# Kernel optimization log

Measured on AMD Instinct MI355X. Metric: run time of the kernel, lower is better.

## Reference

```python
import jax, jax.numpy as jnp
import numpy as np
import math

N, C, H = 2048, 256, 8
D = C // H
T, R, E = 8, 12, 32768
BUCKETS = 21
SEED = 128


def _layernorm(x, g, b, eps=1e-5):
    mu = jnp.mean(x, axis=-1, keepdims=True)
    var = jnp.var(x, axis=-1, keepdims=True)
    return (x - mu) * jax.lax.rsqrt(var + eps) * g + b


def _bucketize_dt(dt, num_buckets):
    eps = 1e-06
    signed_log = jnp.sign(dt) * jnp.log1p(jnp.abs(dt) + eps)
    min_v, max_v = -5.0, 5.0
    norm = (jnp.clip(signed_log, min_v, max_v) - min_v) / (max_v - min_v + 1e-09)
    idx = jnp.floor(norm * (num_buckets - 1)).astype(jnp.int32)
    return jnp.clip(idx, 0, num_buckets - 1)


def setup_inputs() -> dict:
    key = jax.random.key(0)
    ks = jax.random.split(key, 24)
    s = 0.02
    inp = {
        'X': jax.random.normal(ks[0], (N, C), jnp.float32),
        'token_type': jax.random.randint(ks[1], (N,), 0, T, jnp.int32),
        'edge_src': jax.random.randint(ks[2], (E,), 0, N, jnp.int32),
        'edge_dst': jax.random.randint(ks[3], (E,), 0, N, jnp.int32),
        'edge_rel': jax.random.randint(ks[4], (E,), 0, R, jnp.int32),
        'time_vec': jax.random.normal(ks[5], (N,), jnp.float32),
        'seed_count': SEED,
        'Wq': jax.random.normal(ks[6], (C, C), jnp.float32) * s,
        'bq': jnp.zeros((C,), jnp.float32),
        'Wk': jax.random.normal(ks[7], (C, C), jnp.float32) * s,
        'bk': jnp.zeros((C,), jnp.float32),
        'Wv': jax.random.normal(ks[8], (C, C), jnp.float32) * s,
        'bv': jnp.zeros((C,), jnp.float32),
        'Wo': jax.random.normal(ks[9], (C, C), jnp.float32) * s,
        'bo': jnp.zeros((C,), jnp.float32),
        'ln1_g': jnp.ones((C,), jnp.float32),
        'ln1_b': jnp.zeros((C,), jnp.float32),
        'ln2_g': jnp.ones((C,), jnp.float32),
        'ln2_b': jnp.zeros((C,), jnp.float32),
        'W1': jax.random.normal(ks[10], (C, 4 * C), jnp.float32) * s,
        'b1': jnp.zeros((4 * C,), jnp.float32),
        'W2': jax.random.normal(ks[11], (4 * C, C), jnp.float32) * s,
        'b2': jnp.zeros((C,), jnp.float32),
        'adj_rel_bias': jnp.zeros((R, H), jnp.float32),
        'typepair_bias': jnp.zeros((T, T, H), jnp.float32),
        'temp_bias': jax.random.normal(ks[12], (BUCKETS, H), jnp.float32) * s,
    }
    return inp


def reference(X, token_type, edge_src, edge_dst, edge_rel, time_vec, seed_count,
              Wq, bq, Wk, bk, Wv, bv, Wo, bo,
              ln1_g, ln1_b, ln2_g, ln2_b, W1, b1, W2, b2,
              adj_rel_bias, typepair_bias, temp_bias):
    n = X.shape[0]
    h = _layernorm(X, ln1_g, ln1_b)
    q = (h @ Wq + bq).reshape(n, H, D)
    k = (h @ Wk + bk).reshape(n, H, D)
    v = (h @ Wv + bv).reshape(n, H, D)
    scores = jnp.einsum('nhd,mhd->hnm', q, k) / math.sqrt(D)  # [H, N, N]

    # structural bias, factored as [N, N, H] then transposed
    bias = typepair_bias[token_type][:, token_type]            # [N, N, H]
    bias = bias.at[edge_src, edge_dst].add(adj_rel_bias[edge_rel])
    # seed-wise temporal bias on the first seed_count rows
    dt = time_vec[None, :] - time_vec[:seed_count, None]       # [S, N]
    tb = temp_bias[_bucketize_dt(dt, BUCKETS)]                 # [S, N, H]
    bias = bias.at[:seed_count].add(tb)

    attn = jax.nn.softmax(scores + bias.transpose(2, 0, 1), axis=-1)
    o = jnp.einsum('hnm,mhd->nhd', attn, v).reshape(n, C)
    x = X + (o @ Wo + bo)

    h2 = _layernorm(x, ln2_g, ln2_b)
    f = jax.nn.gelu(h2 @ W1 + b1, approximate=False) @ W2 + b2
    return x + f
```

## Files before the change

kernel.cpp:

```cpp
#include <hip/hip_runtime.h>
#include <hip/hip_bf16.h>
#include <math.h>

#define NTOK 2048
#define CDIM 256
#define HHEADS 8
#define DHEAD 32
#define NEDGE 32768
#define NTILE2 32
#define EXTD 64
#define LE 72

typedef __attribute__((ext_vector_type(8))) short short8;
typedef __attribute__((ext_vector_type(4))) short short4v;
typedef __attribute__((ext_vector_type(4))) float f32x4;

static __device__ inline short f2bf(float f) {
    __hip_bfloat16 h = __float2bfloat16(f);
    return *reinterpret_cast<short*>(&h);
}
static __device__ inline float bf2f(short s) {
    unsigned int u = ((unsigned int)(unsigned short)s) << 16;
    return *reinterpret_cast<float*>(&u);
}

__global__ __launch_bounds__(256) void ln4_kernel(const float* __restrict__ X,
    const float* __restrict__ g, const float* __restrict__ b, short* __restrict__ out)
{
    int t = threadIdx.x;
    int wv = t >> 6, lane = t & 63;
    int row = blockIdx.x * 4 + wv;

    float4 x = *(const float4*)&X[(size_t)row * CDIM + lane * 4];
    float s = x.x + x.y + x.z + x.w;
    #pragma unroll
    for (int off = 1; off < 64; off <<= 1) s += __shfl_xor(s, off);
    float mu = s * (1.0f / CDIM);
    float4 d = { x.x - mu, x.y - mu, x.z - mu, x.w - mu };
    float s2 = d.x * d.x + d.y * d.y + d.z * d.z + d.w * d.w;
    #pragma unroll
    for (int off = 1; off < 64; off <<= 1) s2 += __shfl_xor(s2, off);
    float rsig = rsqrtf(s2 * (1.0f / CDIM) + 1e-5f);
    float4 gg = *(const float4*)&g[lane * 4];
    float4 bb = *(const float4*)&b[lane * 4];
    short o4[4];
    o4[0] = f2bf(d.x * rsig * gg.x + bb.x);
    o4[1] = f2bf(d.y * rsig * gg.y + bb.y);
    o4[2] = f2bf(d.z * rsig * gg.z + bb.z);
    o4[3] = f2bf(d.w * rsig * gg.w + bb.w);
    *(short4v*)&out[(size_t)row * CDIM + lane * 4] = *(short4v*)o4;
}

static __device__ inline void transpose_tile_f32(const float* __restrict__ in,
    short* __restrict__ out, int K, int N, int k0, int n0, int t)
{
    __shared__ float tile[64][65];
    int r0 = t >> 4, c0 = (t & 15) * 4;
    #pragma unroll
    for (int i = 0; i < 4; i++) {
        int r = r0 + i * 16;
        float4 v = *(const float4*)(in + (size_t)(k0 + r) * N + n0 + c0);
        tile[r][c0 + 0] = v.x; tile[r][c0 + 1] = v.y;
        tile[r][c0 + 2] = v.z; tile[r][c0 + 3] = v.w;
    }
    __syncthreads();
    #pragma unroll
    for (int i = 0; i < 4; i++) {
        int nr = r0 + i * 16;
        short o4[4];
        #pragma unroll
        for (int j = 0; j < 4; j++) o4[j] = f2bf(tile[c0 + j][nr]);
        *(short4v*)(out + (size_t)(n0 + nr) * K + k0 + c0) = *(short4v*)o4;
    }
}

__global__ __launch_bounds__(256) void prep_kernel(
    const float* __restrict__ Wq, const float* __restrict__ Wk,
    const float* __restrict__ Wv, const float* __restrict__ Wo,
    const float* __restrict__ W1, const float* __restrict__ W2,
    short* __restrict__ wt_qkv, short* __restrict__ wot,
    short* __restrict__ w1t, short* __restrict__ w2t,
    const int* __restrict__ token_type, const float* __restrict__ typepair_bias,
    short* __restrict__ qh, short* __restrict__ kh,
    int* __restrict__ cnt2, float* __restrict__ rowsum)
{
    int b = blockIdx.x;
    int t = threadIdx.x;
    if (b < 192) {
        const float* src; short* dst; int K, N, bx, by;
        if (b < 64) {
            int m = b >> 4, r = b & 15;
            src = (m == 0) ? Wq : (m == 1) ? Wk : (m == 2) ? Wv : Wo;
            dst = (m == 0) ? wt_qkv : (m == 1) ? wt_qkv + 256 * 256
                : (m == 2) ? wt_qkv + 512 * 256 : wot;
            K = 256; N = 256; bx = r & 3; by = r >> 2;
        } else if (b < 128) {
            int r = b - 64; src = W1; dst = w1t; K = 256; N = 1024; bx = r & 15; by = r >> 4;
        } else {
            int r = b - 128; src = W2; dst = w2t; K = 1024; N = 256; bx = r & 3; by = r >> 2;
        }
        transpose_tile_f32(src, dst, K, N, by * 64, bx * 64, t);
    } else if (b < 256) {
        int idx = (b - 192) * 256 + t;
        int row = idx >> 3, h = idx & 7;
        int tt = token_type[row];
        short qe[32], ke[32];
        #pragma unroll
        for (int j = 0; j < 32; j++) {
            if (j < 8) {
                qe[j] = f2bf(typepair_bias[(tt * 8 + j) * 8 + h]);
                ke[j] = (j == tt) ? (short)0x3F80 : (short)0;
            } else { qe[j] = 0; ke[j] = 0; }
        }
        size_t base = ((size_t)h * NTOK + row) * EXTD + 32;
        #pragma unroll
        for (int k = 0; k < 4; k++) {
            *(short8*)&qh[base + k * 8] = *(short8*)&qe[k * 8];
            *(short8*)&kh[base + k * 8] = *(short8*)&ke[k * 8];
        }
    } else if (b < 288) {
        int base = (b - 256) * 2048 + t * 8;
        #pragma unroll
        for (int i = 0; i < 8; i++) cnt2[base + i] = 0;
    } else {
        int base = (b - 288) * 2048 + t * 8;
        #pragma unroll
        for (int i = 0; i < 8; i++) rowsum[base + i] = 0.0f;
    }
}

template<int EPI>
__global__ __launch_bounds__(256) void gemm32_kernel(
    const short* __restrict__ A, const short* __restrict__ Bt,
    const float* __restrict__ bias, const float* __restrict__ resid,
    void* __restrict__ out_, int M, int N, int K)
{
    __shared__ short A_lds[32 * 40];
    __shared__ short B_lds[64 * 40];

    const int t = threadIdx.x;
    const int w = t >> 6, lane = t & 63, c = lane & 15, g = lane >> 4;
    const int row0 = blockIdx.y * 32, col0 = blockIdx.x * 64;
    const int srow = t >> 2, sk = (t & 3) * 8;

    f32x4 acc[2] = {};

    for (int k0 = 0; k0 < K; k0 += 32) {
        if (t < 128)
            *(short8*)&A_lds[srow * 40 + sk] = *(const short8*)&A[(size_t)(row0 + srow) * K + k0 + sk];
        *(short8*)&B_lds[srow * 40 + sk] = *(const short8*)&Bt[(size_t)(col0 + srow) * K + k0 + sk];
        __syncthreads();
        short8 af = *(const short8*)&A_lds[((w & 1) * 16 + c) * 40 + g * 8];
        #pragma unroll
        for (int nf = 0; nf < 2; nf++) {
            short8 bf = *(const short8*)&B_lds[((w >> 1) * 32 + nf * 16 + c) * 40 + g * 8];
            acc[nf] = __builtin_amdgcn_mfma_f32_16x16x32_bf16(af, bf, acc[nf], 0, 0, 0);
        }
        __syncthreads();
    }

    #pragma unroll
    for (int nf = 0; nf < 2; nf++) {
        #pragma unroll
        for (int reg = 0; reg < 4; reg++) {
            int row = row0 + (w & 1) * 16 + g * 4 + reg;
            int col = col0 + (w >> 1) * 32 + nf * 16 + c;
            float v = acc[nf][reg] + bias[col];
            if (EPI == 2) {
                ((float*)out_)[(size_t)row * N + col] = v + resid[(size_t)row * N + col];
            } else {
                v = 0.5f * v * (1.0f + erff(v * 0.70710678118654752f));
                ((short*)out_)[(size_t)row * N + col] = f2bf(v);
            }
        }
    }
}

__global__ __launch_bounds__(256) void gemm32_qkv_kernel(
    const short* __restrict__ A, const short* __restrict__ Bt,
    const float* __restrict__ bq, const float* __restrict__ bk, const float* __restrict__ bv,
    short* __restrict__ qh, short* __restrict__ kh, short* __restrict__ vt)
{
    const int K = CDIM;
    __shared__ short A_lds[32 * 40];
    __shared__ short B_lds[64 * 40];

    const int t = threadIdx.x;
    const int w = t >> 6, lane = t & 63, c = lane & 15, g = lane >> 4;
    const int row0 = blockIdx.y * 32, col0 = blockIdx.x * 64;
    const int srow = t >> 2, sk = (t & 3) * 8;

    f32x4 acc[2] = {};

    for (int k0 = 0; k0 < K; k0 += 32) {
        if (t < 128)
            *(short8*)&A_lds[srow * 40 + sk] = *(const short8*)&A[(size_t)(row0 + srow) * K + k0 + sk];
        *(short8*)&B_lds[srow * 40 + sk] = *(const short8*)&Bt[(size_t)(col0 + srow) * K + k0 + sk];
        __syncthreads();
        short8 af = *(const short8*)&A_lds[((w & 1) * 16 + c) * 40 + g * 8];
        #pragma unroll
        for (int nf = 0; nf < 2; nf++) {
            short8 bf = *(const short8*)&B_lds[((w >> 1) * 32 + nf * 16 + c) * 40 + g * 8];
            acc[nf] = __builtin_amdgcn_mfma_f32_16x16x32_bf16(af, bf, acc[nf], 0, 0, 0);
        }
        __syncthreads();
    }

    const int region = col0 >> 8;
    const int colr0 = col0 & 255;
    const float* bias = (region == 0) ? bq : (region == 1) ? bk : bv;
    #pragma unroll
    for (int nf = 0; nf < 2; nf++) {
        #pragma unroll
        for (int reg = 0; reg < 4; reg++) {
            int row = row0 + (w & 1) * 16 + g * 4 + reg;
            int col = colr0 + (w >> 1) * 32 + nf * 16 + c;
            float v = acc[nf][reg] + bias[col];
            if (region == 0) v *= 0.17677669529663687f;
            short bb = f2bf(v);
            size_t hidx = ((size_t)(col >> 5) * NTOK + row) * EXTD + (col & 31);
            if (region == 0)      qh[hidx] = bb;
            else if (region == 1) kh[hidx] = bb;
            else                  vt[(size_t)col * NTOK + row] = bb;
        }
    }
}

__global__ void edge_hist2_kernel(const int* __restrict__ src, const int* __restrict__ dst,
    int* __restrict__ cnt, int E)
{
    int e = blockIdx.x * blockDim.x + threadIdx.x;
    if (e < E) atomicAdd(&cnt[src[e] * NTILE2 + (dst[e] >> 6)], 1);
}

__global__ __launch_bounds__(256) void edge_scan2_kernel(const int* __restrict__ cnt,
    int* __restrict__ row_ptr, int* __restrict__ wcur)
{
    __shared__ int sums[256];
    int t = threadIdx.x;
    int base = t * 256;
    int s = 0;
    for (int i = 0; i < 256; i++) s += cnt[base + i];
    sums[t] = s;
    __syncthreads();
    for (int off = 1; off < 256; off <<= 1) {
        int v = (t >= off) ? sums[t - off] : 0;
        __syncthreads();
        sums[t] += v;
        __syncthreads();
    }
    int run = (t == 0) ? 0 : sums[t - 1];
    for (int i = 0; i < 256; i++) {
        row_ptr[base + i] = run;
        wcur[base + i] = run;
        run += cnt[base + i];
    }
    if (t == 255) row_ptr[NTOK * NTILE2] = run;
}

__global__ void edge_scatter2_kernel(const int* __restrict__ src, const int* __restrict__ dst,
    const int* __restrict__ rel, int* __restrict__ wcur, int2* __restrict__ pairs, int E)
{
    int e = blockIdx.x * blockDim.x + threadIdx.x;
    if (e < E) {
        int d = dst[e];
        int pos = atomicAdd(&wcur[src[e] * NTILE2 + (d >> 6)], 1);
        pairs[pos] = make_int2(d, rel[e]);
    }
}

__global__ __launch_bounds__(256) void sgemm_exp_kernel(
    const short* __restrict__ qh, const short* __restrict__ kh,
    const float* __restrict__ time_vec, const int* __restrict__ seed_ptr,
    const float* __restrict__ adj_rel_bias, const float* __restrict__ temp_bias,
    const int* __restrict__ row_ptr2, const int2* __restrict__ pairs2,
    short* __restrict__ S, float* __restrict__ rowsum)
{
    __shared__ short A_lds[64 * LE];
    __shared__ short B_lds[64 * LE];
    __shared__ float tcol_s[64];
    __shared__ float temp_h[21];
    __shared__ float adj_h[12];

    const int t = threadIdx.x;
    const int w = t >> 6, lane = t & 63, c = lane & 15, g = lane >> 4;
    const int h = blockIdx.z;
    const int m0 = blockIdx.x * 64, n0 = blockIdx.y * 64;
    const int seed = seed_ptr[0];

    {
        int r = t >> 3, off = (t & 7) * 8;
        *(short8*)&A_lds[r * LE + off] =
            *(const short8*)&qh[((size_t)h * NTOK + n0 + r) * EXTD + off];
        *(short8*)&A_lds[(r + 32) * LE + off] =
            *(const short8*)&qh[((size_t)h * NTOK + n0 + 32 + r) * EXTD + off];
        *(short8*)&B_lds[r * LE + off] =
            *(const short8*)&kh[((size_t)h * NTOK + m0 + r) * EXTD + off];
        *(short8*)&B_lds[(r + 32) * LE + off] =
            *(const short8*)&kh[((size_t)h * NTOK + m0 + 32 + r) * EXTD + off];
    }
    if (t < 64) tcol_s[t] = time_vec[m0 + t];
    if (t < 21) temp_h[t] = temp_bias[t * HHEADS + h];
    if (t < 12) adj_h[t] = adj_rel_bias[t * HHEADS + h];
    __syncthreads();

    short8 alo = *(const short8*)&A_lds[(w * 16 + c) * LE + g * 8];
    short8 ahi = *(const short8*)&A_lds[(w * 16 + c) * LE + 32 + g * 8];
    f32x4 acc[4] = {};
    #pragma unroll
    for (int nf = 0; nf < 4; nf++) {
        short8 blo = *(const short8*)&B_lds[(nf * 16 + c) * LE + g * 8];
        short8 bhi = *(const short8*)&B_lds[(nf * 16 + c) * LE + 32 + g * 8];
        acc[nf] = __builtin_amdgcn_mfma_f32_16x16x32_bf16(alo, blo, acc[nf], 0, 0, 0);
        acc[nf] = __builtin_amdgcn_mfma_f32_16x16x32_bf16(ahi, bhi, acc[nf], 0, 0, 0);
    }

    #pragma unroll
    for (int reg = 0; reg < 4; reg++) {
        const int rloc = w * 16 + g * 4 + reg;
        const int n = n0 + rloc;
        const bool rowTemp = (n < seed);
        const float tn = time_vec[n];

        {
            int bidx = n * NTILE2 + (m0 >> 6);
            int e0 = row_ptr2[bidx], e1 = row_ptr2[bidx + 1];
            for (int e = e0; e < e1; ++e) {
                int2 pr = pairs2[e];
                int cl = pr.x & 63;
                if ((cl & 15) == c) {
                    float ab = adj_h[pr.y];
                    int nfi = cl >> 4;
                    #pragma unroll
                    for (int nf = 0; nf < 4; nf++)
                        if (nf == nfi) acc[nf][reg] += ab;
                }
            }
        }

        float rsum = 0.0f;
        short p4[4];
        #pragma unroll
        for (int nf = 0; nf < 4; nf++) {
            float s = acc[nf][reg];
            if (rowTemp) {
                float dt = tcol_s[nf * 16 + c] - tn;
                float ab = fabsf(dt) + 1e-6f;
                float sg = (dt > 0.0f) ? 1.0f : ((dt < 0.0f) ? -1.0f : 0.0f);
                float sl = sg * log1pf(ab);
                sl = fminf(fmaxf(sl, -5.0f), 5.0f);
                float norm = (sl + 5.0f) * (1.0f / (10.0f + 1e-9f));
                int bidx = (int)floorf(norm * 20.0f);
                bidx = min(max(bidx, 0), 20);
                s += temp_h[bidx];
            }
            float e = __expf(s);
            rsum += e;
            p4[nf] = f2bf(e);
        }
        #pragma unroll
        for (int nf = 0; nf < 4; nf++)
            S[((size_t)h * NTOK + n) * NTOK + m0 + nf * 16 + c] = p4[nf];
        rsum += __shfl_xor(rsum, 1);
        rsum += __shfl_xor(rsum, 2);
        rsum += __shfl_xor(rsum, 4);
        rsum += __shfl_xor(rsum, 8);
        if (c == 0) atomicAdd(&rowsum[h * NTOK + n], rsum);
    }
}

__global__ __launch_bounds__(256) void pv_kernel(
    const short* __restrict__ P, const short* __restrict__ vt,
    const float* __restrict__ rowsum, short* __restrict__ o)
{
    __shared__ short A_lds[32 * LE];
    __shared__ short B_lds[32 * LE];
    const int t = threadIdx.x;
    const int w = t >> 6, lane = t & 63, c = lane & 15, g = lane >> 4;
    const int h = blockIdx.y;
    const int n0 = blockIdx.x * 32;
    const int rowblk = (w & 1) * 16, colblk = (w >> 1) * 16;

    f32x4 acc = {0.0f, 0.0f, 0.0f, 0.0f};

    for (int k0 = 0; k0 < NTOK; k0 += 64) {
        int r = t >> 3, off = (t & 7) * 8;
        *(short8*)&A_lds[r * LE + off] =
            *(const short8*)&P[((size_t)h * NTOK + n0 + r) * NTOK + k0 + off];
        *(short8*)&B_lds[r * LE + off] =
            *(const short8*)&vt[(size_t)(h * 32 + r) * NTOK + k0 + off];
        __syncthreads();
        short8 alo = *(const short8*)&A_lds[(rowblk + c) * LE + g * 8];
        short8 ahi = *(const short8*)&A_lds[(rowblk + c) * LE + 32 + g * 8];
        short8 blo = *(const short8*)&B_lds[(colblk + c) * LE + g * 8];
        short8 bhi = *(const short8*)&B_lds[(colblk + c) * LE + 32 + g * 8];
        acc = __builtin_amdgcn_mfma_f32_16x16x32_bf16(alo, blo, acc, 0, 0, 0);
        acc = __builtin_amdgcn_mfma_f32_16x16x32_bf16(ahi, bhi, acc, 0, 0, 0);
        __syncthreads();
    }

    #pragma unroll
    for (int reg = 0; reg < 4; reg++) {
        int row = n0 + rowblk + g * 4 + reg;
        int col = h * 32 + colblk + c;
        float inv = 1.0f / rowsum[h * NTOK + row];
        o[(size_t)row * CDIM + col] = f2bf(acc[reg] * inv);
    }
}

extern "C" void kernel_launch(void* const* d_in, const int* in_sizes, int n_in,
                              void* d_out, int out_size, void* d_ws, size_t ws_size,
                              hipStream_t stream)
{
    (void)in_sizes; (void)n_in; (void)out_size; (void)ws_size;
    const float* X        = (const float*)d_in[0];
    const int* token_type = (const int*)d_in[1];
    const int* edge_src   = (const int*)d_in[2];
    const int* edge_dst   = (const int*)d_in[3];
    const int* edge_rel   = (const int*)d_in[4];
    const float* time_vec = (const float*)d_in[5];
    const int* seed_ptr   = (const int*)d_in[6];
    const float* Wq = (const float*)d_in[7];  const float* bq = (const float*)d_in[8];
    const float* Wk = (const float*)d_in[9];  const float* bk = (const float*)d_in[10];
    const float* Wv = (const float*)d_in[11]; const float* bv = (const float*)d_in[12];
    const float* Wo = (const float*)d_in[13]; const float* bo = (const float*)d_in[14];
    const float* ln1_g = (const float*)d_in[15]; const float* ln1_b = (const float*)d_in[16];
    const float* ln2_g = (const float*)d_in[17]; const float* ln2_b = (const float*)d_in[18];
    const float* W1 = (const float*)d_in[19]; const float* b1 = (const float*)d_in[20];
    const float* W2 = (const float*)d_in[21]; const float* b2 = (const float*)d_in[22];
    const float* adj_rel_bias  = (const float*)d_in[23];
    const float* typepair_bias = (const float*)d_in[24];
    const float* temp_bias     = (const float*)d_in[25];
    float* out = (float*)d_out;

    char* base = (char*)d_ws;
    size_t off = 0;
    auto alloc = [&](size_t bytes) { char* p = base + off; off += (bytes + 255) & ~(size_t)255; return p; };
    short* qh_bf   = (short*)alloc((size_t)HHEADS * NTOK * EXTD * 2);
    short* kh_bf   = (short*)alloc((size_t)HHEADS * NTOK * EXTD * 2);
    short* vt_bf   = (short*)alloc((size_t)256 * NTOK * 2);
    short* h1_bf   = (short*)alloc((size_t)NTOK * 256 * 2);
    short* h2_bf   = (short*)alloc((size_t)NTOK * 256 * 2);
    short* o_bf    = (short*)alloc((size_t)NTOK * 256 * 2);
    short* mid_bf  = (short*)alloc((size_t)NTOK * 1024 * 2);
    float* xb      = (float*)alloc((size_t)NTOK * 256 * 4);
    short* wt_qkv  = (short*)alloc((size_t)768 * 256 * 2);
    short* wot     = (short*)alloc((size_t)256 * 256 * 2);
    short* w1t     = (short*)alloc((size_t)1024 * 256 * 2);
    short* w2t     = (short*)alloc((size_t)256 * 1024 * 2);
    int2*  pairs2  = (int2*)alloc((size_t)NEDGE * 8);
    int*   cnt2    = (int*)alloc((size_t)NTOK * NTILE2 * 4);
    int*   rowptr2 = (int*)alloc(((size_t)NTOK * NTILE2 + 1) * 4);
    int*   wcur2   = (int*)alloc((size_t)NTOK * NTILE2 * 4);
    float* rowsum  = (float*)alloc((size_t)HHEADS * NTOK * 4);
    short* S       = (short*)alloc((size_t)HHEADS * NTOK * NTOK * 2);

    prep_kernel<<<296, 256, 0, stream>>>(Wq, Wk, Wv, Wo, W1, W2,
                                         wt_qkv, wot, w1t, w2t,
                                         token_type, typepair_bias,
                                         qh_bf, kh_bf, cnt2, rowsum);

    edge_hist2_kernel<<<NEDGE / 256, 256, 0, stream>>>(edge_src, edge_dst, cnt2, NEDGE);
    edge_scan2_kernel<<<1, 256, 0, stream>>>(cnt2, rowptr2, wcur2);
    edge_scatter2_kernel<<<NEDGE / 256, 256, 0, stream>>>(edge_src, edge_dst, edge_rel, wcur2, pairs2, NEDGE);

    ln4_kernel<<<NTOK / 4, 256, 0, stream>>>(X, ln1_g, ln1_b, h1_bf);

    gemm32_qkv_kernel<<<dim3(12, 64), 256, 0, stream>>>(h1_bf, wt_qkv, bq, bk, bv,
                                                        qh_bf, kh_bf, vt_bf);

    sgemm_exp_kernel<<<dim3(32, 32, 8), 256, 0, stream>>>(
        qh_bf, kh_bf, time_vec, seed_ptr, adj_rel_bias, temp_bias,
        rowptr2, pairs2, S, rowsum);
    pv_kernel<<<dim3(64, 8), 256, 0, stream>>>(S, vt_bf, rowsum, o_bf);

    gemm32_kernel<2><<<dim3(4, 64), 256, 0, stream>>>(o_bf, wot, bo, X, xb, NTOK, 256, 256);

    ln4_kernel<<<NTOK / 4, 256, 0, stream>>>(xb, ln2_g, ln2_b, h2_bf);

    gemm32_kernel<3><<<dim3(16, 64), 256, 0, stream>>>(h2_bf, w1t, b1, nullptr, mid_bf, NTOK, 1024, 256);
    gemm32_kernel<2><<<dim3(4, 64), 256, 0, stream>>>(mid_bf, w2t, b2, xb, out, NTOK, 256, 1024);
}
```

Measured before the change: 161.7 us.

## Permute S and V columns for vectorized stores, vectorize edge scan, cache row pointers

The P matrix columns within each 64-wide tile are stored in a permuted order so each lane writes its four probabilities as one 8-byte store, and V's transposed rows are permuted the same way so the PV product stays consistent. The edge prefix scan reads and writes int4 vectors. The per-row edge CSR pointers are preloaded into shared memory, and the time_vec load is skipped for non-seed rows. This cuts scattered 2-byte global stores and redundant global loads in the score kernel, but relies on the permutation matching exactly between the S writer and the V writer.

```diff
diff --git a/kernel.cpp b/kernel.cpp
--- a/kernel.cpp
+++ b/kernel.cpp
@@ -221,7 +221,11 @@
             size_t hidx = ((size_t)(col >> 5) * NTOK + row) * EXTD + (col & 31);
             if (region == 0)      qh[hidx] = bb;
             else if (region == 1) kh[hidx] = bb;
-            else                  vt[(size_t)col * NTOK + row] = bb;
+            else {
+                int rl = row & 63;
+                int rp = ((rl & 15) << 2) | (rl >> 4);
+                vt[(size_t)col * NTOK + (row & ~63) + rp] = bb;
+            }
         }
     }
 }
@@ -240,7 +244,10 @@
     int t = threadIdx.x;
     int base = t * 256;
     int s = 0;
-    for (int i = 0; i < 256; i++) s += cnt[base + i];
+    for (int i = 0; i < 64; i++) {
+        int4 v = *(const int4*)&cnt[base + i * 4];
+        s += v.x + v.y + v.z + v.w;
+    }
     sums[t] = s;
     __syncthreads();
     for (int off = 1; off < 256; off <<= 1) {
@@ -250,10 +257,15 @@
         __syncthreads();
     }
     int run = (t == 0) ? 0 : sums[t - 1];
-    for (int i = 0; i < 256; i++) {
-        row_ptr[base + i] = run;
-        wcur[base + i] = run;
-        run += cnt[base + i];
+    for (int i = 0; i < 64; i++) {
+        int4 v = *(const int4*)&cnt[base + i * 4];
+        int4 o;
+        o.x = run; run += v.x;
+        o.y = run; run += v.y;
+        o.z = run; run += v.z;
+        o.w = run; run += v.w;
+        *(int4*)&row_ptr[base + i * 4] = o;
+        *(int4*)&wcur[base + i * 4] = o;
     }
     if (t == 255) row_ptr[NTOK * NTILE2] = run;
 }
@@ -281,6 +293,7 @@
     __shared__ float tcol_s[64];
     __shared__ float temp_h[21];
     __shared__ float adj_h[12];
+    __shared__ int rpA[64], rpB[64];
 
     const int t = threadIdx.x;
     const int w = t >> 6, lane = t & 63, c = lane & 15, g = lane >> 4;
@@ -299,7 +312,12 @@
         *(short8*)&B_lds[(r + 32) * LE + off] =
             *(const short8*)&kh[((size_t)h * NTOK + m0 + 32 + r) * EXTD + off];
     }
-    if (t < 64) tcol_s[t] = time_vec[m0 + t];
+    if (t < 64) {
+        tcol_s[t] = time_vec[m0 + t];
+        int bidx = (n0 + t) * NTILE2 + (m0 >> 6);
+        rpA[t] = row_ptr2[bidx];
+        rpB[t] = row_ptr2[bidx + 1];
+    }
     if (t < 21) temp_h[t] = temp_bias[t * HHEADS + h];
     if (t < 12) adj_h[t] = adj_rel_bias[t * HHEADS + h];
     __syncthreads();
@@ -320,11 +338,10 @@
         const int rloc = w * 16 + g * 4 + reg;
         const int n = n0 + rloc;
         const bool rowTemp = (n < seed);
-        const float tn = time_vec[n];
+        const float tn = rowTemp ? time_vec[n] : 0.0f;
 
         {
-            int bidx = n * NTILE2 + (m0 >> 6);
-            int e0 = row_ptr2[bidx], e1 = row_ptr2[bidx + 1];
+            int e0 = rpA[rloc], e1 = rpB[rloc];
             for (int e = e0; e < e1; ++e) {
                 int2 pr = pairs2[e];
                 int cl = pr.x & 63;
@@ -358,9 +375,7 @@
             rsum += e;
             p4[nf] = f2bf(e);
         }
-        #pragma unroll
-        for (int nf = 0; nf < 4; nf++)
-            S[((size_t)h * NTOK + n) * NTOK + m0 + nf * 16 + c] = p4[nf];
+        *(short4v*)&S[((size_t)h * NTOK + n) * NTOK + m0 + c * 4] = *(short4v*)p4;
         rsum += __shfl_xor(rsum, 1);
         rsum += __shfl_xor(rsum, 2);
         rsum += __shfl_xor(rsum, 4);
@@ -450,7 +465,7 @@
     short* w2t     = (short*)alloc((size_t)256 * 1024 * 2);
     int2*  pairs2  = (int2*)alloc((size_t)NEDGE * 8);
     int*   cnt2    = (int*)alloc((size_t)NTOK * NTILE2 * 4);
-    int*   rowptr2 = (int*)alloc(((size_t)NTOK * NTILE2 + 1) * 4);
+    int*   rowptr2 = (int*)alloc(((size_t)NTOK * NTILE2 + 4) * 4);
     int*   wcur2   = (int*)alloc((size_t)NTOK * NTILE2 * 4);
     float* rowsum  = (float*)alloc((size_t)HHEADS * NTOK * 4);
     short* S       = (short*)alloc((size_t)HHEADS * NTOK * NTOK * 2);
```

Result: faster. 156.8 us (-3.0%).
